# Optimization experiments

Hardware: AMD Instinct MI355X
Metric: run time of the kernel (lower is better)

Reference implementation:

```python
import jax, jax.numpy as jnp
import numpy as np

N, F, H, D, E, G = 50000, 64, 4, 64, 800000, 64
NEG_SLOPE = 0.2


def setup_inputs() -> dict:
    key = jax.random.key(0)
    ks = jax.random.split(key, 10)
    return {
        "x": jax.random.normal(ks[0], (N, F), jnp.float32),
        "mask": jax.random.uniform(ks[1], (N, F), jnp.float32),
        "edge_index": jax.random.randint(ks[2], (2, E), 0, N, jnp.int64),
        "batch_idx": jnp.sort(jax.random.randint(ks[3], (N,), 0, G, jnp.int64)),
        "W_gat": jax.random.normal(ks[4], (H * D, F), jnp.float32) * 0.05,
        "att_src": jax.random.normal(ks[5], (H, D), jnp.float32) * 0.05,
        "att_dst": jax.random.normal(ks[6], (H, D), jnp.float32) * 0.05,
        "bias_gat": jax.random.normal(ks[7], (H * D,), jnp.float32) * 0.05,
        "W_lin": jax.random.normal(ks[8], (D, H * D), jnp.float32) * 0.05,
        "b_lin": jax.random.normal(ks[9], (D,), jnp.float32) * 0.05,
    }


def reference(x, mask, edge_index, batch_idx, W_gat, att_src, att_dst, bias_gat, W_lin, b_lin):
    n = x.shape[0]
    row, col = edge_index[0], edge_index[1]

    # ---- get_mask(mask, edge_index, hops=1): scatter_add(mask[col] -> row), threshold
    m = jax.ops.segment_sum(mask[col], row, num_segments=n)
    m = (m > 0).astype(x.dtype)  # [N, F]

    # ---- GATConv(x, edge_index): add self loops (PyG default)
    loop = jnp.arange(n, dtype=edge_index.dtype)
    src = jnp.concatenate([edge_index[0], loop])  # source j
    dst = jnp.concatenate([edge_index[1], loop])  # target i

    xw = (x @ W_gat.T).reshape(n, H, D)  # per-head projection [N,H,D]
    a_s = jnp.einsum("nhd,hd->nh", xw, att_src)  # [N,H]
    a_d = jnp.einsum("nhd,hd->nh", xw, att_dst)
    e = jax.nn.leaky_relu(a_s[src] + a_d[dst], NEG_SLOPE)  # [E+N, H]

    # segment softmax over incoming edges of each destination node
    emax = jax.ops.segment_max(e, dst, num_segments=n)  # [N,H]
    ex = jnp.exp(e - emax[dst])
    denom = jax.ops.segment_sum(ex, dst, num_segments=n)
    alpha = ex / (denom[dst] + 1e-16)  # [E+N, H]

    out = jax.ops.segment_sum(alpha[:, :, None] * xw[src], dst, num_segments=n)
    out = out.reshape(n, H * D) + bias_gat  # concat heads + bias

    # ---- mask expand to heads and fuse: x = linear(x * mask)
    mexp = jnp.broadcast_to(m[:, None, :], (n, H, F)).reshape(n, H * F)
    out = (out * mexp) @ W_lin.T + b_lin  # [N, D]

    # ---- GraphSizeNorm: divide by sqrt(#nodes in each graph)
    deg = jax.ops.segment_sum(jnp.ones((n,), x.dtype), batch_idx, num_segments=G)
    inv_sqrt = jnp.where(deg > 0, deg, 1.0) ** -0.5
    out = out * inv_sqrt[batch_idx][:, None]
    return out
```

## Files before the change

### kernel.cpp

```cpp
#include <hip/hip_runtime.h>
#include <cstdint>
#include <math.h>

constexpr float NEG_SLOPE = 0.2f;

__device__ __forceinline__ float lrelu(float v) { return v > 0.0f ? v : NEG_SLOPE * v; }

__device__ __forceinline__ unsigned short f2bf(float f) {
    uint32_t u = __float_as_uint(f);
    uint32_t r = (u + 0x7fffu + ((u >> 16) & 1u)) >> 16;
    return (unsigned short)r;
}
__device__ __forceinline__ float bf2f(unsigned short v) { return __uint_as_float((uint32_t)v << 16); }
__device__ __forceinline__ float bflo(uint32_t v) { return __uint_as_float(v << 16); }
__device__ __forceinline__ float bfhi(uint32_t v) { return __uint_as_float(v & 0xffff0000u); }

typedef short bf16x8 __attribute__((ext_vector_type(8)));
typedef float f32x4 __attribute__((ext_vector_type(4)));

__global__ void k_init(const float* __restrict__ mask,
                       unsigned long long* __restrict__ mbits,
                       unsigned long long* __restrict__ magg,
                       int* __restrict__ deg, int* __restrict__ startg, int N)
{
    if (blockIdx.x == 0 && threadIdx.x < 64) startg[threadIdx.x] = N;
    int wid  = (blockIdx.x * blockDim.x + threadIdx.x) >> 6;
    int lane = threadIdx.x & 63;
    if (wid >= N) return;
    float v = mask[(size_t)wid * 64 + lane];
    unsigned long long b = __ballot(v > 0.0f);
    if (lane == 0) { mbits[wid] = b; magg[wid] = 0ULL; deg[wid] = 0; }
}

__global__ void k_edge_prep(const int* __restrict__ ei,
                            const unsigned long long* __restrict__ mbits,
                            unsigned long long* __restrict__ magg,
                            int* __restrict__ deg, int E)
{
    int e = blockIdx.x * blockDim.x + threadIdx.x;
    if (e >= E) return;
    int r = ei[e];
    int c = ei[E + e];
    unsigned long long b = mbits[c];
    if ((magg[r] & b) != b) atomicOr(magg + r, b);
    atomicAdd(deg + c, 1);
}

__global__ void k_vprep(const float* __restrict__ Wg,
                        const float* __restrict__ att_s, const float* __restrict__ att_d,
                        float* __restrict__ vs, float* __restrict__ vd)
{
    int t = threadIdx.x;
    int h = t >> 6, k = t & 63;
    float s = 0.f, d = 0.f;
    for (int dd = 0; dd < 64; ++dd) {
        float w = Wg[(size_t)(h * 64 + dd) * 64 + k];
        s += w * att_s[h * 64 + dd];
        d += w * att_d[h * 64 + dd];
    }
    vs[t] = s; vd[t] = d;
}

__launch_bounds__(256)
__global__ void k_att(const float* __restrict__ x,
                      const float* __restrict__ vs, const float* __restrict__ vd,
                      float* __restrict__ a_s, float* __restrict__ a_d, int N)
{
    __shared__ float4 vsm[128];
    int tid = threadIdx.x;
    if (tid < 64) vsm[tid] = ((const float4*)vs)[tid];
    else if (tid < 128) vsm[tid] = ((const float4*)vd)[tid - 64];
    __syncthreads();
    int i = blockIdx.x * 256 + tid;
    if (i >= N) return;
    const float4* xr = (const float4*)(x + (size_t)i * 64);
    float s0=0,s1=0,s2=0,s3=0, d0=0,d1=0,d2=0,d3=0;
    #pragma unroll
    for (int q = 0; q < 16; ++q) {
        float4 xv = xr[q];
        float4 a0 = vsm[q], a1 = vsm[16+q], a2 = vsm[32+q], a3 = vsm[48+q];
        float4 c0 = vsm[64+q], c1 = vsm[80+q], c2 = vsm[96+q], c3 = vsm[112+q];
        s0 += xv.x*a0.x + xv.y*a0.y + xv.z*a0.z + xv.w*a0.w;
        s1 += xv.x*a1.x + xv.y*a1.y + xv.z*a1.z + xv.w*a1.w;
        s2 += xv.x*a2.x + xv.y*a2.y + xv.z*a2.z + xv.w*a2.w;
        s3 += xv.x*a3.x + xv.y*a3.y + xv.z*a3.z + xv.w*a3.w;
        d0 += xv.x*c0.x + xv.y*c0.y + xv.z*c0.z + xv.w*c0.w;
        d1 += xv.x*c1.x + xv.y*c1.y + xv.z*c1.z + xv.w*c1.w;
        d2 += xv.x*c2.x + xv.y*c2.y + xv.z*c2.z + xv.w*c2.w;
        d3 += xv.x*c3.x + xv.y*c3.y + xv.z*c3.z + xv.w*c3.w;
    }
    *(float4*)&a_s[(size_t)i * 4] = make_float4(s0, s1, s2, s3);
    *(float4*)&a_d[(size_t)i * 4] = make_float4(d0, d1, d2, d3);
}

__launch_bounds__(256)
__global__ void k_gemm1m(const float* __restrict__ x, const float* __restrict__ Wg,
                         const int* __restrict__ batch_idx,
                         uint32_t* __restrict__ xwp, int* __restrict__ startg, int N)
{
    __shared__ __align__(16) uint32_t AsH[2048];
    __shared__ __align__(16) uint32_t AsL[2048];
    __shared__ __align__(16) uint32_t BsH[8192];
    const int tid = threadIdx.x;
    const int r0  = blockIdx.x * 64;

    for (int idx = tid; idx < 2048; idx += 256) {
        int r = idx >> 5, k2 = idx & 31;
        float2 v = make_float2(0.f, 0.f);
        if (r0 + r < N) v = *(const float2*)&x[(size_t)(r0 + r) * 64 + 2 * k2];
        unsigned short h0 = f2bf(v.x), h1 = f2bf(v.y);
        unsigned short l0 = f2bf(v.x - bf2f(h0)), l1 = f2bf(v.y - bf2f(h1));
        int di = (r * 32 + k2) ^ ((r & 7) << 2);
        AsH[di] = (uint32_t)h0 | ((uint32_t)h1 << 16);
        AsL[di] = (uint32_t)l0 | ((uint32_t)l1 << 16);
    }
    for (int idx = tid; idx < 8192; idx += 256) {
        int c = idx >> 5, k2 = idx & 31;
        float2 v = *(const float2*)&Wg[(size_t)c * 64 + 2 * k2];
        int di = (c * 32 + k2) ^ ((c & 7) << 2);
        BsH[di] = (uint32_t)f2bf(v.x) | ((uint32_t)f2bf(v.y) << 16);
    }
    if (tid < 64 && (r0 + tid) < N) {
        int i = r0 + tid;
        int b = batch_idx[i];
        int pb = (i > 0) ? batch_idx[i - 1] : -1;
        if (b != pb) startg[b] = i;
    }
    __syncthreads();

    const int lane = tid & 63;
    const int wv   = tid >> 6;
    const int rl   = lane & 15;
    const int kg   = lane >> 4;
    const int ct0  = (wv & 1) * 2 + (wv >> 1) * 8;
    const int swz  = (rl & 7) << 2;

    f32x4 acc[4][4];
    #pragma unroll
    for (int r = 0; r < 4; ++r)
        #pragma unroll
        for (int cs = 0; cs < 4; ++cs) acc[r][cs] = (f32x4){0.f, 0.f, 0.f, 0.f};

    #pragma unroll
    for (int ks = 0; ks < 2; ++ks) {
        bf16x8 aH[4], aL[4], bH[4];
        #pragma unroll
        for (int r = 0; r < 4; ++r) {
            int ui = (((r * 16 + rl) * 32) + ks * 16 + kg * 4) ^ swz;
            aH[r] = *(const bf16x8*)&AsH[ui];
            aL[r] = *(const bf16x8*)&AsL[ui];
        }
        #pragma unroll
        for (int cs = 0; cs < 4; ++cs) {
            int ct = ct0 + (cs & 1) + (cs >> 1) * 4;
            int ui = (((ct * 16 + rl) * 32) + ks * 16 + kg * 4) ^ swz;
            bH[cs] = *(const bf16x8*)&BsH[ui];
        }
        #pragma unroll
        for (int r = 0; r < 4; ++r)
            #pragma unroll
            for (int cs = 0; cs < 4; ++cs) {
                acc[r][cs] = __builtin_amdgcn_mfma_f32_16x16x32_bf16(aH[r], bH[cs], acc[r][cs], 0, 0, 0);
                acc[r][cs] = __builtin_amdgcn_mfma_f32_16x16x32_bf16(aL[r], bH[cs], acc[r][cs], 0, 0, 0);
            }
    }

    #pragma unroll
    for (int r = 0; r < 4; ++r) {
        #pragma unroll
        for (int reg = 0; reg < 4; ++reg) {
            int row = r0 + r * 16 + kg * 4 + reg;
            if (row < N) {
                #pragma unroll
                for (int p = 0; p < 2; ++p) {
                    int c_lo = (ct0 + p) * 16 + rl;
                    int wrd  = ((c_lo >> 7) << 6) | (c_lo & 63);
                    uint32_t lo = f2bf(acc[r][p][reg]);
                    uint32_t hi = f2bf(acc[r][p + 2][reg]);
                    xwp[(size_t)row * 128 + wrd] = lo | (hi << 16);
                }
            }
        }
    }
}

__global__ void k_scan1(const int* __restrict__ deg, int* __restrict__ off,
                        int* __restrict__ bsum, int N)
{
    __shared__ int s[256];
    int t = threadIdx.x;
    int i = blockIdx.x * 256 + t;
    int v = (i < N) ? deg[i] : 0;
    s[t] = v; __syncthreads();
    for (int o = 1; o < 256; o <<= 1) {
        int u = (t >= o) ? s[t - o] : 0;
        __syncthreads();
        s[t] += u;
        __syncthreads();
    }
    int incl = s[t];
    if (i < N) off[i] = incl - v;
    if (t == 255) bsum[blockIdx.x] = incl;
}

__global__ void k_scan2(const int* __restrict__ bsum, int* __restrict__ bpre,
                        int* __restrict__ off, const int* __restrict__ startg,
                        float* __restrict__ invs, int NB, int N)
{
    __shared__ int s[256];
    int t = threadIdx.x;
    int v = (t < NB) ? bsum[t] : 0;
    s[t] = v; __syncthreads();
    for (int o = 1; o < 256; o <<= 1) {
        int u = (t >= o) ? s[t - o] : 0;
        __syncthreads();
        s[t] += u;
        __syncthreads();
    }
    if (t < NB) bpre[t] = s[t] - v;
    if (t == 255) off[N] = s[255];
    if (t < 64) {
        int st = startg[t];
        int en = N;
        for (int g2 = t + 1; g2 < 64; ++g2) en = min(en, startg[g2]);
        int d = en - st;
        float dv = (d > 0) ? (float)d : 1.0f;
        invs[t] = 1.0f / sqrtf(dv);
    }
}

__global__ void k_scan3(int* __restrict__ off, int* __restrict__ cursor,
                        const int* __restrict__ bpre, int N)
{
    int i = blockIdx.x * blockDim.x + threadIdx.x;
    if (i >= N) return;
    int v = off[i] + bpre[blockIdx.x];
    off[i] = v;
    cursor[i] = v;
}

__global__ void k_fill(const int* __restrict__ ei, int* __restrict__ cursor,
                       int* __restrict__ csr, int E)
{
    int e = blockIdx.x * blockDim.x + threadIdx.x;
    if (e >= E) return;
    int r = ei[e];
    int c = ei[E + e];
    int pos = atomicAdd(cursor + c, 1);
    csr[pos] = r;
}

__launch_bounds__(256)
__global__ void k_main4(const uint32_t* __restrict__ xwp,
                        const float* __restrict__ a_s,
                        const float* __restrict__ a_d,
                        const int* __restrict__ off,
                        const int* __restrict__ csr,
                        const unsigned long long* __restrict__ magg,
                        const float* __restrict__ bias,
                        float* __restrict__ tb, int N)
{
    const int bid   = blockIdx.x;
    const int xcd   = bid & 7;
    const int phase = (xcd >= 4) ? 1 : 0;
    const int pblk  = (bid >> 3) * 4 + (xcd & 3);
    const int lane  = threadIdx.x & 63;
    const int wv    = threadIdx.x >> 6;
    const int wid   = pblk * 4 + wv;
    const int nw    = 8192;

    const int fbase = phase * 128;
    const float b0c = bias[fbase + lane];
    const float b1c = bias[fbase + 64 + lane];
    const uint32_t* base = xwp + (size_t)phase * 64 + lane;

    for (int i = wid; i < N; i += nw) {
        const int beg = off[i], end = off[i + 1];
        const float2 ad2 = *(const float2*)(a_d + (size_t)i * 4 + phase * 2);
        const float2 as2 = *(const float2*)(a_s + (size_t)i * 4 + phase * 2);
        const float exa = __expf(lrelu(as2.x + ad2.x));
        const float exb = __expf(lrelu(as2.y + ad2.y));

        uint32_t sv = base[(size_t)i * 128];
        float accA0 = exa * bflo(sv), accA1 = exb * bfhi(sv);
        float accB0 = 0.f, accB1 = 0.f, accC0 = 0.f, accC1 = 0.f, accD0 = 0.f, accD1 = 0.f;
        float s0 = 0.f, s1 = 0.f;

        for (int kc = beg; kc < end; kc += 64) {
            const int cnt = min(64, end - kc);
            int sreg = 0; float e0 = 0.f, e1 = 0.f;
            if (lane < cnt) {
                sreg = csr[kc + lane];
                const float2 g = *(const float2*)(a_s + (size_t)sreg * 4 + phase * 2);
                e0 = __expf(lrelu(g.x + ad2.x));
                e1 = __expf(lrelu(g.y + ad2.y));
            }
            s0 += e0; s1 += e1;

            int j = 0;
            for (; j + 4 <= cnt; j += 4) {
                int sA = __shfl(sreg, j    ), sB = __shfl(sreg, j + 1);
                int sC = __shfl(sreg, j + 2), sD = __shfl(sreg, j + 3);
                float wA0 = __shfl(e0, j    ), wA1 = __shfl(e1, j    );
                float wB0 = __shfl(e0, j + 1), wB1 = __shfl(e1, j + 1);
                float wC0 = __shfl(e0, j + 2), wC1 = __shfl(e1, j + 2);
                float wD0 = __shfl(e0, j + 3), wD1 = __shfl(e1, j + 3);
                uint32_t vA = base[(size_t)sA * 128];
                uint32_t vB = base[(size_t)sB * 128];
                uint32_t vC = base[(size_t)sC * 128];
                uint32_t vD = base[(size_t)sD * 128];
                accA0 += wA0 * bflo(vA); accA1 += wA1 * bfhi(vA);
                accB0 += wB0 * bflo(vB); accB1 += wB1 * bfhi(vB);
                accC0 += wC0 * bflo(vC); accC1 += wC1 * bfhi(vC);
                accD0 += wD0 * bflo(vD); accD1 += wD1 * bfhi(vD);
            }
            for (; j < cnt; ++j) {
                int   s  = __shfl(sreg, j);
                float w0 = __shfl(e0, j);
                float w1 = __shfl(e1, j);
                uint32_t v = base[(size_t)s * 128];
                accA0 += w0 * bflo(v);
                accA1 += w1 * bfhi(v);
            }
        }
        float acc0 = (accA0 + accB0) + (accC0 + accD0);
        float acc1 = (accA1 + accB1) + (accC1 + accD1);
        #pragma unroll
        for (int o = 1; o < 64; o <<= 1) { s0 += __shfl_xor(s0, o); s1 += __shfl_xor(s1, o); }
        s0 += exa; s1 += exb;
        const float r0 = 1.0f / (s0 + 1e-16f);
        const float r1 = 1.0f / (s1 + 1e-16f);

        const unsigned long long mb = magg[i];
        const float mbit = (float)((mb >> lane) & 1ULL);
        const size_t ob = (size_t)i * 256 + fbase + lane;
        tb[ob     ] = (acc0 * r0 + b0c) * mbit;
        tb[ob + 64] = (acc1 * r1 + b1c) * mbit;
    }
}

__launch_bounds__(256, 4)
__global__ void k_gemm2r(const float* __restrict__ tb, const float* __restrict__ Wl,
                         const float* __restrict__ bl,
                         const int* __restrict__ batch_idx, const float* __restrict__ invs,
                         float* __restrict__ out, int N)
{
    __shared__ float ts[32 * 256];
    const int tid  = threadIdx.x;
    const int wv   = tid >> 6;
    const int lane = tid & 63;
    const int cl   = lane & 15;
    const int q    = lane >> 4;
    const int c    = wv * 16 + cl;
    const int r0   = blockIdx.x * 32;

    float4 w4[16];
    #pragma unroll
    for (int m = 0; m < 8; ++m) {
        w4[m*2+0] = *(const float4*)&Wl[(size_t)c * 256 + m*32 + q*8 + 0];
        w4[m*2+1] = *(const float4*)&Wl[(size_t)c * 256 + m*32 + q*8 + 4];
    }
    const float blc = bl[c];

    const float4* tb4 = (const float4*)tb;
    float4* ts4 = (float4*)ts;
    #pragma unroll
    for (int it = 0; it < 8; ++it) {
        int idx = tid + it * 256;
        int row = idx >> 6;
        float4 v = make_float4(0.f, 0.f, 0.f, 0.f);
        if (r0 + row < N) v = tb4[(size_t)r0 * 64 + idx];
        ts4[idx] = v;
    }
    __syncthreads();

    #pragma unroll
    for (int rb = 0; rb < 32; rb += 4) {
        float p[4];
        #pragma unroll
        for (int rr = 0; rr < 4; ++rr) {
            const float4* tr = ts4 + (rb + rr) * 64 + q * 2;
            float a = 0.f;
            #pragma unroll
            for (int m = 0; m < 8; ++m) {
                float4 t0 = tr[m*8 + 0];
                float4 t1 = tr[m*8 + 1];
                float4 u0 = w4[m*2+0], u1 = w4[m*2+1];
                a += t0.x*u0.x + t0.y*u0.y + t0.z*u0.z + t0.w*u0.w
                   + t1.x*u1.x + t1.y*u1.y + t1.z*u1.z + t1.w*u1.w;
            }
            a += __shfl_xor(a, 16);
            a += __shfl_xor(a, 32);
            p[rr] = a;
        }
        int rr  = lane >> 4;
        float val = (rr == 0) ? p[0] : (rr == 1) ? p[1] : (rr == 2) ? p[2] : p[3];
        int row = r0 + rb + rr;
        if (row < N) {
            float sc = invs[batch_idx[row]];
            out[(size_t)row * 64 + c] = (val + blc) * sc;
        }
    }
}

extern "C" void kernel_launch(void* const* d_in, const int* in_sizes, int n_in,
                              void* d_out, int out_size, void* d_ws, size_t ws_size,
                              hipStream_t stream)
{
    const float* x      = (const float*)d_in[0];
    const float* mask   = (const float*)d_in[1];
    const int*   ei     = (const int*)d_in[2];
    const int*   batch  = (const int*)d_in[3];
    const float* Wg     = (const float*)d_in[4];
    const float* att_s  = (const float*)d_in[5];
    const float* att_d  = (const float*)d_in[6];
    const float* bias_g = (const float*)d_in[7];
    const float* Wl     = (const float*)d_in[8];
    const float* bl     = (const float*)d_in[9];
    float* out = (float*)d_out;

    const int N = in_sizes[0] / 64;
    const int E = in_sizes[2] / 2;

    char* w = (char*)d_ws;
    auto alloc = [&](size_t bytes) { char* p = w; w += (bytes + 255) & ~(size_t)255; return p; };
    uint32_t* xwp  = (uint32_t*)alloc((size_t)N * 128 * 4);
    float* tbuf  = (float*)alloc((size_t)N * 256 * 4);
    float* a_s   = (float*)alloc((size_t)N * 4 * 4);
    float* a_d   = (float*)alloc((size_t)N * 4 * 4);
    unsigned long long* mbits = (unsigned long long*)alloc((size_t)N * 8);
    unsigned long long* magg  = (unsigned long long*)alloc((size_t)N * 8);
    int* deg    = (int*)alloc((size_t)N * 4);
    int* off    = (int*)alloc((size_t)(N + 1) * 4);
    int* cursor = (int*)alloc((size_t)N * 4);
    int* csr    = (int*)alloc((size_t)E * 4);
    int* bsum   = (int*)alloc(256 * 4);
    int* bpre   = (int*)alloc(256 * 4);
    int* startg = (int*)alloc(64 * 4);
    float* invs = (float*)alloc(64 * 4);
    float* vs   = (float*)alloc(256 * 4);
    float* vd   = (float*)alloc(256 * 4);

    int nbN4  = (N + 3) / 4;
    int nb256 = (N + 255) / 256;

    k_init<<<nbN4, 256, 0, stream>>>(mask, mbits, magg, deg, startg, N);
    k_edge_prep<<<(E + 255) / 256, 256, 0, stream>>>(ei, mbits, magg, deg, E);
    k_vprep<<<1, 256, 0, stream>>>(Wg, att_s, att_d, vs, vd);
    k_att<<<nb256, 256, 0, stream>>>(x, vs, vd, a_s, a_d, N);
    k_gemm1m<<<(N + 63) / 64, 256, 0, stream>>>(x, Wg, batch, xwp, startg, N);
    k_scan1<<<nb256, 256, 0, stream>>>(deg, off, bsum, N);
    k_scan2<<<1, 256, 0, stream>>>(bsum, bpre, off, startg, invs, nb256, N);
    k_scan3<<<nb256, 256, 0, stream>>>(off, cursor, bpre, N);
    k_fill<<<(E + 255) / 256, 256, 0, stream>>>(ei, cursor, csr, E);
    k_main4<<<4096, 256, 0, stream>>>(xwp, a_s, a_d, off, csr, magg, bias_g, tbuf, N);
    k_gemm2r<<<(N + 31) / 32, 256, 0, stream>>>(tbuf, Wl, bl, batch, invs, out, N);
}
```

Before: 277.8 us.

## Process all heads per wave in aggregation and use split-bf16 MFMA for output GEMM

The edge aggregation kernel now handles all four heads of a node in one wave. Each lane gathers a uint2 of the packed bf16 features, and neighbor indices and weights are staged through LDS instead of lane shuffles. This halves the number of passes over CSR indices and a_s lookups. The final linear layer is rewritten as a 64-row tile MFMA GEMM using a hi/lo bf16 split (three products) to keep near-fp32 accuracy. The attention-vector precompute kernel is folded into the attention kernel, so each block recomputes it at the cost of redundant small work.

Measured after the change: 259.3 us. 6.7% less time.

```diff
diff --git a/kernel.cpp b/kernel.cpp
--- a/kernel.cpp
+++ b/kernel.cpp
@@ -46,30 +46,24 @@
     atomicAdd(deg + c, 1);
 }
 
-__global__ void k_vprep(const float* __restrict__ Wg,
-                        const float* __restrict__ att_s, const float* __restrict__ att_d,
-                        float* __restrict__ vs, float* __restrict__ vd)
-{
-    int t = threadIdx.x;
-    int h = t >> 6, k = t & 63;
-    float s = 0.f, d = 0.f;
-    for (int dd = 0; dd < 64; ++dd) {
-        float w = Wg[(size_t)(h * 64 + dd) * 64 + k];
-        s += w * att_s[h * 64 + dd];
-        d += w * att_d[h * 64 + dd];
-    }
-    vs[t] = s; vd[t] = d;
-}
-
 __launch_bounds__(256)
-__global__ void k_att(const float* __restrict__ x,
-                      const float* __restrict__ vs, const float* __restrict__ vd,
-                      float* __restrict__ a_s, float* __restrict__ a_d, int N)
-{
-    __shared__ float4 vsm[128];
+__global__ void k_att2(const float* __restrict__ x, const float* __restrict__ Wg,
+                       const float* __restrict__ att_s, const float* __restrict__ att_d,
+                       float* __restrict__ a_s, float* __restrict__ a_d, int N)
+{
+    __shared__ float vs_l[256];
+    __shared__ float vd_l[256];
     int tid = threadIdx.x;
-    if (tid < 64) vsm[tid] = ((const float4*)vs)[tid];
-    else if (tid < 128) vsm[tid] = ((const float4*)vd)[tid - 64];
+    {
+        int h = tid >> 6, k = tid & 63;
+        float s = 0.f, d = 0.f;
+        for (int dd = 0; dd < 64; ++dd) {
+            float w = Wg[(size_t)(h * 64 + dd) * 64 + k];
+            s += w * att_s[h * 64 + dd];
+            d += w * att_d[h * 64 + dd];
+        }
+        vs_l[tid] = s; vd_l[tid] = d;
+    }
     __syncthreads();
     int i = blockIdx.x * 256 + tid;
     if (i >= N) return;
@@ -78,8 +72,14 @@
     #pragma unroll
     for (int q = 0; q < 16; ++q) {
         float4 xv = xr[q];
-        float4 a0 = vsm[q], a1 = vsm[16+q], a2 = vsm[32+q], a3 = vsm[48+q];
-        float4 c0 = vsm[64+q], c1 = vsm[80+q], c2 = vsm[96+q], c3 = vsm[112+q];
+        float4 a0 = *(const float4*)&vs_l[4*q];
+        float4 a1 = *(const float4*)&vs_l[64 + 4*q];
+        float4 a2 = *(const float4*)&vs_l[128 + 4*q];
+        float4 a3 = *(const float4*)&vs_l[192 + 4*q];
+        float4 c0 = *(const float4*)&vd_l[4*q];
+        float4 c1 = *(const float4*)&vd_l[64 + 4*q];
+        float4 c2 = *(const float4*)&vd_l[128 + 4*q];
+        float4 c3 = *(const float4*)&vd_l[192 + 4*q];
         s0 += xv.x*a0.x + xv.y*a0.y + xv.z*a0.z + xv.w*a0.w;
         s1 += xv.x*a1.x + xv.y*a1.y + xv.z*a1.z + xv.w*a1.w;
         s2 += xv.x*a2.x + xv.y*a2.y + xv.z*a2.z + xv.w*a2.w;
@@ -251,7 +251,7 @@
 }
 
 __launch_bounds__(256)
-__global__ void k_main4(const uint32_t* __restrict__ xwp,
+__global__ void k_main5(const uint32_t* __restrict__ xwp,
                         const float* __restrict__ a_s,
                         const float* __restrict__ a_d,
                         const int* __restrict__ off,
@@ -260,145 +260,173 @@
                         const float* __restrict__ bias,
                         float* __restrict__ tb, int N)
 {
-    const int bid   = blockIdx.x;
-    const int xcd   = bid & 7;
-    const int phase = (xcd >= 4) ? 1 : 0;
-    const int pblk  = (bid >> 3) * 4 + (xcd & 3);
-    const int lane  = threadIdx.x & 63;
-    const int wv    = threadIdx.x >> 6;
-    const int wid   = pblk * 4 + wv;
-    const int nw    = 8192;
-
-    const int fbase = phase * 128;
-    const float b0c = bias[fbase + lane];
-    const float b1c = bias[fbase + 64 + lane];
-    const uint32_t* base = xwp + (size_t)phase * 64 + lane;
+    __shared__ __align__(16) uint32_t su[4][64];
+    __shared__ float2 e01s[4][64];
+    __shared__ float2 e23s[4][64];
+
+    const int lane = threadIdx.x & 63;
+    const int wv   = threadIdx.x >> 6;
+    const int wid  = blockIdx.x * 4 + wv;
+    const int nw   = gridDim.x * 4;
+    const int hp   = lane >> 5;
+    const int d0   = (lane & 31) * 2;
+
+    const uint2* xw2 = (const uint2*)xwp;
+    const float2 bsL = *(const float2*)&bias[hp * 128 + d0];
+    const float2 bsH = *(const float2*)&bias[hp * 128 + 64 + d0];
+    const float2* ep = hp ? e23s[wv] : e01s[wv];
 
     for (int i = wid; i < N; i += nw) {
         const int beg = off[i], end = off[i + 1];
-        const float2 ad2 = *(const float2*)(a_d + (size_t)i * 4 + phase * 2);
-        const float2 as2 = *(const float2*)(a_s + (size_t)i * 4 + phase * 2);
-        const float exa = __expf(lrelu(as2.x + ad2.x));
-        const float exb = __expf(lrelu(as2.y + ad2.y));
-
-        uint32_t sv = base[(size_t)i * 128];
-        float accA0 = exa * bflo(sv), accA1 = exb * bfhi(sv);
-        float accB0 = 0.f, accB1 = 0.f, accC0 = 0.f, accC1 = 0.f, accD0 = 0.f, accD1 = 0.f;
-        float s0 = 0.f, s1 = 0.f;
+        const float4 adv = *(const float4*)(a_d + (size_t)i * 4);
+        const float4 asv = *(const float4*)(a_s + (size_t)i * 4);
+        const float ex0 = __expf(lrelu(asv.x + adv.x));
+        const float ex1 = __expf(lrelu(asv.y + adv.y));
+        const float ex2 = __expf(lrelu(asv.z + adv.z));
+        const float ex3 = __expf(lrelu(asv.w + adv.w));
+
+        const uint2 sv = xw2[(size_t)i * 64 + lane];
+        const float wls = hp ? ex2 : ex0;
+        const float whs = hp ? ex3 : ex1;
+        float accL0 = wls * bflo(sv.x), accH0 = whs * bfhi(sv.x);
+        float accL1 = wls * bflo(sv.y), accH1 = whs * bfhi(sv.y);
+        float s0 = 0.f, s1 = 0.f, s2 = 0.f, s3 = 0.f;
 
         for (int kc = beg; kc < end; kc += 64) {
             const int cnt = min(64, end - kc);
-            int sreg = 0; float e0 = 0.f, e1 = 0.f;
+            uint32_t sreg = 0; float e0 = 0.f, e1 = 0.f, e2 = 0.f, e3 = 0.f;
             if (lane < cnt) {
                 sreg = csr[kc + lane];
-                const float2 g = *(const float2*)(a_s + (size_t)sreg * 4 + phase * 2);
-                e0 = __expf(lrelu(g.x + ad2.x));
-                e1 = __expf(lrelu(g.y + ad2.y));
-            }
-            s0 += e0; s1 += e1;
+                const float4 g = *(const float4*)(a_s + (size_t)sreg * 4);
+                e0 = __expf(lrelu(g.x + adv.x));
+                e1 = __expf(lrelu(g.y + adv.y));
+                e2 = __expf(lrelu(g.z + adv.z));
+                e3 = __expf(lrelu(g.w + adv.w));
+            }
+            s0 += e0; s1 += e1; s2 += e2; s3 += e3;
+            su[wv][lane]   = sreg;
+            e01s[wv][lane] = make_float2(e0, e1);
+            e23s[wv][lane] = make_float2(e2, e3);
 
             int j = 0;
             for (; j + 4 <= cnt; j += 4) {
-                int sA = __shfl(sreg, j    ), sB = __shfl(sreg, j + 1);
-                int sC = __shfl(sreg, j + 2), sD = __shfl(sreg, j + 3);
-                float wA0 = __shfl(e0, j    ), wA1 = __shfl(e1, j    );
-                float wB0 = __shfl(e0, j + 1), wB1 = __shfl(e1, j + 1);
-                float wC0 = __shfl(e0, j + 2), wC1 = __shfl(e1, j + 2);
-                float wD0 = __shfl(e0, j + 3), wD1 = __shfl(e1, j + 3);
-                uint32_t vA = base[(size_t)sA * 128];
-                uint32_t vB = base[(size_t)sB * 128];
-                uint32_t vC = base[(size_t)sC * 128];
-                uint32_t vD = base[(size_t)sD * 128];
-                accA0 += wA0 * bflo(vA); accA1 += wA1 * bfhi(vA);
-                accB0 += wB0 * bflo(vB); accB1 += wB1 * bfhi(vB);
-                accC0 += wC0 * bflo(vC); accC1 += wC1 * bfhi(vC);
-                accD0 += wD0 * bflo(vD); accD1 += wD1 * bfhi(vD);
+                uint4 sq = *(const uint4*)&su[wv][j];
+                float2 wA = ep[j], wB = ep[j+1], wC = ep[j+2], wD = ep[j+3];
+                uint2 vA = xw2[(size_t)sq.x * 64 + lane];
+                uint2 vB = xw2[(size_t)sq.y * 64 + lane];
+                uint2 vC = xw2[(size_t)sq.z * 64 + lane];
+                uint2 vD = xw2[(size_t)sq.w * 64 + lane];
+                accL0 += wA.x * bflo(vA.x); accH0 += wA.y * bfhi(vA.x);
+                accL1 += wA.x * bflo(vA.y); accH1 += wA.y * bfhi(vA.y);
+                accL0 += wB.x * bflo(vB.x); accH0 += wB.y * bfhi(vB.x);
+                accL1 += wB.x * bflo(vB.y); accH1 += wB.y * bfhi(vB.y);
+                accL0 += wC.x * bflo(vC.x); accH0 += wC.y * bfhi(vC.x);
+                accL1 += wC.x * bflo(vC.y); accH1 += wC.y * bfhi(vC.y);
+                accL0 += wD.x * bflo(vD.x); accH0 += wD.y * bfhi(vD.x);
+                accL1 += wD.x * bflo(vD.y); accH1 += wD.y * bfhi(vD.y);
             }
             for (; j < cnt; ++j) {
-                int   s  = __shfl(sreg, j);
-                float w0 = __shfl(e0, j);
-                float w1 = __shfl(e1, j);
-                uint32_t v = base[(size_t)s * 128];
-                accA0 += w0 * bflo(v);
-                accA1 += w1 * bfhi(v);
-            }
-        }
-        float acc0 = (accA0 + accB0) + (accC0 + accD0);
-        float acc1 = (accA1 + accB1) + (accC1 + accD1);
-        #pragma unroll
-        for (int o = 1; o < 64; o <<= 1) { s0 += __shfl_xor(s0, o); s1 += __shfl_xor(s1, o); }
-        s0 += exa; s1 += exb;
-        const float r0 = 1.0f / (s0 + 1e-16f);
-        const float r1 = 1.0f / (s1 + 1e-16f);
+                uint32_t s = su[wv][j];
+                float2 wE = ep[j];
+                uint2 v = xw2[(size_t)s * 64 + lane];
+                accL0 += wE.x * bflo(v.x); accH0 += wE.y * bfhi(v.x);
+                accL1 += wE.x * bflo(v.y); accH1 += wE.y * bfhi(v.y);
+            }
+        }
+        #pragma unroll
+        for (int o = 1; o < 64; o <<= 1) {
+            s0 += __shfl_xor(s0, o); s1 += __shfl_xor(s1, o);
+            s2 += __shfl_xor(s2, o); s3 += __shfl_xor(s3, o);
+        }
+        s0 += ex0; s1 += ex1; s2 += ex2; s3 += ex3;
+        const float slo = hp ? s2 : s0;
+        const float shi = hp ? s3 : s1;
+        const float rlo = 1.0f / (slo + 1e-16f);
+        const float rhi = 1.0f / (shi + 1e-16f);
 
         const unsigned long long mb = magg[i];
-        const float mbit = (float)((mb >> lane) & 1ULL);
-        const size_t ob = (size_t)i * 256 + fbase + lane;
-        tb[ob     ] = (acc0 * r0 + b0c) * mbit;
-        tb[ob + 64] = (acc1 * r1 + b1c) * mbit;
-    }
-}
-
-__launch_bounds__(256, 4)
-__global__ void k_gemm2r(const float* __restrict__ tb, const float* __restrict__ Wl,
+        const float m0 = (float)((mb >> d0) & 1ULL);
+        const float m1 = (float)((mb >> (d0 + 1)) & 1ULL);
+        float2 oL = make_float2((accL0 * rlo + bsL.x) * m0, (accL1 * rlo + bsL.y) * m1);
+        float2 oH = make_float2((accH0 * rhi + bsH.x) * m0, (accH1 * rhi + bsH.y) * m1);
+        *(float2*)&tb[(size_t)i * 256 + hp * 128 + d0]      = oL;
+        *(float2*)&tb[(size_t)i * 256 + hp * 128 + 64 + d0] = oH;
+    }
+}
+
+__launch_bounds__(256)
+__global__ void k_gemm2m(const float* __restrict__ tb, const float* __restrict__ Wl,
                          const float* __restrict__ bl,
                          const int* __restrict__ batch_idx, const float* __restrict__ invs,
                          float* __restrict__ out, int N)
 {
-    __shared__ float ts[32 * 256];
-    const int tid  = threadIdx.x;
+    __shared__ __align__(16) uint32_t AH[2048];
+    __shared__ __align__(16) uint32_t AL[2048];
+    __shared__ __align__(16) uint32_t BH[2048];
+    __shared__ __align__(16) uint32_t BL[2048];
+    const int tid = threadIdx.x;
+    const int r0  = blockIdx.x * 64;
+    const int lane = tid & 63;
     const int wv   = tid >> 6;
-    const int lane = tid & 63;
-    const int cl   = lane & 15;
-    const int q    = lane >> 4;
-    const int c    = wv * 16 + cl;
-    const int r0   = blockIdx.x * 32;
-
-    float4 w4[16];
-    #pragma unroll
-    for (int m = 0; m < 8; ++m) {
-        w4[m*2+0] = *(const float4*)&Wl[(size_t)c * 256 + m*32 + q*8 + 0];
-        w4[m*2+1] = *(const float4*)&Wl[(size_t)c * 256 + m*32 + q*8 + 4];
-    }
-    const float blc = bl[c];
-
-    const float4* tb4 = (const float4*)tb;
-    float4* ts4 = (float4*)ts;
-    #pragma unroll
-    for (int it = 0; it < 8; ++it) {
-        int idx = tid + it * 256;
-        int row = idx >> 6;
-        float4 v = make_float4(0.f, 0.f, 0.f, 0.f);
-        if (r0 + row < N) v = tb4[(size_t)r0 * 64 + idx];
-        ts4[idx] = v;
-    }
-    __syncthreads();
-
-    #pragma unroll
-    for (int rb = 0; rb < 32; rb += 4) {
-        float p[4];
-        #pragma unroll
-        for (int rr = 0; rr < 4; ++rr) {
-            const float4* tr = ts4 + (rb + rr) * 64 + q * 2;
-            float a = 0.f;
+    const int rl   = lane & 15;
+    const int kg   = lane >> 4;
+    const int swz  = (rl & 7) << 2;
+
+    f32x4 acc[4];
+    #pragma unroll
+    for (int r = 0; r < 4; ++r) acc[r] = (f32x4){0.f, 0.f, 0.f, 0.f};
+
+    for (int kc = 0; kc < 4; ++kc) {
+        if (kc) __syncthreads();
+        for (int idx = tid; idx < 2048; idx += 256) {
+            int r = idx >> 5, k2 = idx & 31;
+            float2 v = make_float2(0.f, 0.f);
+            if (r0 + r < N) v = *(const float2*)&tb[(size_t)(r0 + r) * 256 + kc * 64 + 2 * k2];
+            unsigned short h0 = f2bf(v.x), h1 = f2bf(v.y);
+            unsigned short l0 = f2bf(v.x - bf2f(h0)), l1 = f2bf(v.y - bf2f(h1));
+            int di = (r * 32 + k2) ^ ((r & 7) << 2);
+            AH[di] = (uint32_t)h0 | ((uint32_t)h1 << 16);
+            AL[di] = (uint32_t)l0 | ((uint32_t)l1 << 16);
+        }
+        for (int idx = tid; idx < 2048; idx += 256) {
+            int c = idx >> 5, k2 = idx & 31;
+            float2 v = *(const float2*)&Wl[(size_t)c * 256 + kc * 64 + 2 * k2];
+            unsigned short h0 = f2bf(v.x), h1 = f2bf(v.y);
+            unsigned short l0 = f2bf(v.x - bf2f(h0)), l1 = f2bf(v.y - bf2f(h1));
+            int di = (c * 32 + k2) ^ ((c & 7) << 2);
+            BH[di] = (uint32_t)h0 | ((uint32_t)h1 << 16);
+            BL[di] = (uint32_t)l0 | ((uint32_t)l1 << 16);
+        }
+        __syncthreads();
+
+        #pragma unroll
+        for (int ks = 0; ks < 2; ++ks) {
+            int uib = ((wv * 16 + rl) * 32 + ks * 16 + kg * 4) ^ swz;
+            bf16x8 bHf = *(const bf16x8*)&BH[uib];
+            bf16x8 bLf = *(const bf16x8*)&BL[uib];
             #pragma unroll
-            for (int m = 0; m < 8; ++m) {
-                float4 t0 = tr[m*8 + 0];
-                float4 t1 = tr[m*8 + 1];
-                float4 u0 = w4[m*2+0], u1 = w4[m*2+1];
-                a += t0.x*u0.x + t0.y*u0.y + t0.z*u0.z + t0.w*u0.w
-                   + t1.x*u1.x + t1.y*u1.y + t1.z*u1.z + t1.w*u1.w;
-            }
-            a += __shfl_xor(a, 16);
-            a += __shfl_xor(a, 32);
-            p[rr] = a;
-        }
-        int rr  = lane >> 4;
-        float val = (rr == 0) ? p[0] : (rr == 1) ? p[1] : (rr == 2) ? p[2] : p[3];
-        int row = r0 + rb + rr;
-        if (row < N) {
-            float sc = invs[batch_idx[row]];
-            out[(size_t)row * 64 + c] = (val + blc) * sc;
+            for (int r = 0; r < 4; ++r) {
+                int ui = ((r * 16 + rl) * 32 + ks * 16 + kg * 4) ^ swz;
+                bf16x8 aHf = *(const bf16x8*)&AH[ui];
+                bf16x8 aLf = *(const bf16x8*)&AL[ui];
+                acc[r] = __builtin_amdgcn_mfma_f32_16x16x32_bf16(aHf, bHf, acc[r], 0, 0, 0);
+                acc[r] = __builtin_amdgcn_mfma_f32_16x16x32_bf16(aHf, bLf, acc[r], 0, 0, 0);
+                acc[r] = __builtin_amdgcn_mfma_f32_16x16x32_bf16(aLf, bHf, acc[r], 0, 0, 0);
+            }
+        }
+    }
+
+    const int col = wv * 16 + rl;
+    const float blc = bl[col];
+    #pragma unroll
+    for (int r = 0; r < 4; ++r) {
+        #pragma unroll
+        for (int reg = 0; reg < 4; ++reg) {
+            int row = r0 + r * 16 + kg * 4 + reg;
+            if (row < N) {
+                float sc = invs[batch_idx[row]];
+                out[(size_t)row * 64 + col] = (acc[r][reg] + blc) * sc;
+            }
         }
     }
 }
@@ -438,21 +466,18 @@
     int* bpre   = (int*)alloc(256 * 4);
     int* startg = (int*)alloc(64 * 4);
     float* invs = (float*)alloc(64 * 4);
-    float* vs   = (float*)alloc(256 * 4);
-    float* vd   = (float*)alloc(256 * 4);
 
     int nbN4  = (N + 3) / 4;
     int nb256 = (N + 255) / 256;
 
     k_init<<<nbN4, 256, 0, stream>>>(mask, mbits, magg, deg, startg, N);
     k_edge_prep<<<(E + 255) / 256, 256, 0, stream>>>(ei, mbits, magg, deg, E);
-    k_vprep<<<1, 256, 0, stream>>>(Wg, att_s, att_d, vs, vd);
-    k_att<<<nb256, 256, 0, stream>>>(x, vs, vd, a_s, a_d, N);
+    k_att2<<<nb256, 256, 0, stream>>>(x, Wg, att_s, att_d, a_s, a_d, N);
     k_gemm1m<<<(N + 63) / 64, 256, 0, stream>>>(x, Wg, batch, xwp, startg, N);
     k_scan1<<<nb256, 256, 0, stream>>>(deg, off, bsum, N);
     k_scan2<<<1, 256, 0, stream>>>(bsum, bpre, off, startg, invs, nb256, N);
     k_scan3<<<nb256, 256, 0, stream>>>(off, cursor, bpre, N);
     k_fill<<<(E + 255) / 256, 256, 0, stream>>>(ei, cursor, csr, E);
-    k_main4<<<4096, 256, 0, stream>>>(xwp, a_s, a_d, off, csr, magg, bias_g, tbuf, N);
-    k_gemm2r<<<(N + 31) / 32, 256, 0, stream>>>(tbuf, Wl, bl, batch, invs, out, N);
-}
+    k_main5<<<2048, 256, 0, stream>>>(xwp, a_s, a_d, off, csr, magg, bias_g, tbuf, N);
+    k_gemm2m<<<(N + 63) / 64, 256, 0, stream>>>(tbuf, Wl, bl, batch, invs, out, N);
+}
```
